# Kernel tuning notes

Hardware: AMD Instinct MI355X
Metric: run time of the kernel (lower is better)

The kernel has to match this reference:

```python
import jax, jax.numpy as jnp
import numpy as np

TAU = 2.0       # LIF membrane time constant
V_TH = 1.0      # spike threshold
ALPHA = 2.0     # ATan surrogate sharpness
EPS = 1e-5      # BatchNorm eps


@jax.custom_vjp
def spike_fn(x):
    return (x >= 0.0).astype(x.dtype)

def _spike_fwd(x):
    return spike_fn(x), x

def _spike_bwd(x, g):
    # ATan surrogate: alpha/2 / (1 + (pi/2 * alpha * x)^2)
    sg = (ALPHA / 2.0) / (1.0 + (jnp.pi / 2.0 * ALPHA * x) ** 2)
    return (g * sg,)

spike_fn.defvjp(_spike_fwd, _spike_bwd)


def lif_multistep(x):
    # x: [T, B, C, L]; spikingjelly LIFNode, decay_input=True, hard reset to 0,
    # detach_reset=True (spike detached in the reset path only).
    def step(v, xt):
        v = v + (xt - v) / TAU
        s = spike_fn(v - V_TH)
        v = (1.0 - jax.lax.stop_gradient(s)) * v
        return v, s
    v0 = jnp.zeros_like(x[0])
    _, spks = jax.lax.scan(step, v0, x)
    return spks  # [T, B, C, L]


def delta_encoder(inputs, bn_gamma, bn_beta, enc_w, enc_b):
    # inputs: [B, L, C]
    delta = jnp.concatenate(
        [jnp.zeros_like(inputs[:, :1]), inputs[:, 1:] - inputs[:, :-1]], axis=1
    )  # [B, L, C]
    d = jnp.transpose(delta, (0, 2, 1))[:, None]  # [B, 1, C, L]
    # BatchNorm2d(1), training mode: stats over all elements (single channel)
    mean = jnp.mean(d)
    var = jnp.var(d)
    d = (d - mean) * jax.lax.rsqrt(var + EPS) * bn_gamma[0] + bn_beta[0]
    d = jnp.transpose(d, (0, 2, 3, 1))  # [B, C, L, 1]
    # Linear(1, T): enc[b,c,l,t] = d[b,c,l,0] * w[t,0] + b[t]
    enc = d * enc_w[:, 0] + enc_b  # [B, C, L, T]
    enc = jnp.transpose(enc, (3, 0, 1, 2))  # [T, B, C, L]
    spks = lif_multistep(enc)
    return jnp.transpose(spks, (1, 0, 2, 3))  # [B, T, C, L]


def setup_inputs() -> dict:
    key = jax.random.key(0)
    k1, k2, k3 = jax.random.split(key, 3)
    B, L, C, T = 32, 4096, 8, 64
    inputs = jax.random.normal(k1, (B, L, C), dtype=jnp.float32)
    bn_gamma = jnp.ones((1,), dtype=jnp.float32)
    bn_beta = jnp.zeros((1,), dtype=jnp.float32)
    # torch Linear(1, T) init: U(-1, 1) since fan_in = 1
    enc_w = jax.random.uniform(k2, (T, 1), dtype=jnp.float32, minval=-1.0, maxval=1.0)
    enc_b = jax.random.uniform(k3, (T,), dtype=jnp.float32, minval=-1.0, maxval=1.0)
    return {"inputs": inputs, "bn_gamma": bn_gamma, "bn_beta": bn_beta,
            "enc_w": enc_w, "enc_b": enc_b}


def reference(inputs, bn_gamma, bn_beta, enc_w, enc_b):
    return delta_encoder(inputs, bn_gamma, bn_beta, enc_w, enc_b)
```

## Files before the change

### kernel.cpp

```cpp
#include <hip/hip_runtime.h>
#include <math.h>

#define NBATCH 32
#define NL     4096
#define NC     8
#define NT     64
#define NTOT   (NBATCH * NL * NC)

typedef float f32x4 __attribute__((ext_vector_type(4)));

__global__ __launch_bounds__(256) void reduce_kernel(const float* __restrict__ in,
                                                     double* __restrict__ part) {
    __shared__ double sm[256], sm2[256];
    const int tid = threadIdx.x;
    double s = 0.0, s2 = 0.0;
    for (int i = blockIdx.x * 256 + tid; i < NTOT; i += 256 * 256) {
        double d = 0.0;
        if ((i & (NL * NC - 1)) >= NC) {
            d = (double)in[i] - (double)in[i - NC];
        }
        s  += d;
        s2 += d * d;
    }
    sm[tid] = s; sm2[tid] = s2;
    __syncthreads();
    for (int off = 128; off > 0; off >>= 1) {
        if (tid < off) { sm[tid] += sm[tid + off]; sm2[tid] += sm2[tid + off]; }
        __syncthreads();
    }
    if (tid == 0) {
        part[2 * blockIdx.x]     = sm[0];
        part[2 * blockIdx.x + 1] = sm2[0];
    }
}

__global__ __launch_bounds__(256) void finalize_kernel(const double* __restrict__ part,
                                                       const float* __restrict__ gamma,
                                                       const float* __restrict__ beta,
                                                       const float* __restrict__ wv,
                                                       const float* __restrict__ bv,
                                                       double2* __restrict__ pq) {
    __shared__ double sm[256], sm2[256];
    __shared__ double sAB[2];
    const int tid = threadIdx.x;
    sm[tid]  = part[2 * tid];
    sm2[tid] = part[2 * tid + 1];
    __syncthreads();
    for (int off = 128; off > 0; off >>= 1) {
        if (tid < off) { sm[tid] += sm[tid + off]; sm2[tid] += sm2[tid + off]; }
        __syncthreads();
    }
    if (tid == 0) {
        const double mean = sm[0] / (double)NTOT;
        const double var  = sm2[0] / (double)NTOT - mean * mean;
        const double inv  = 1.0 / sqrt(var + 1e-5);
        const double A    = inv * (double)gamma[0];
        const double Bc   = (double)beta[0] - mean * A;
        sAB[0] = A;
        sAB[1] = Bc;
    }
    __syncthreads();
    if (tid < NT) {
        const double A  = sAB[0];
        const double Bc = sAB[1];
        const double w  = (double)wv[tid];
        const double b  = (double)bv[tid];
        double2 r;
        r.x = 0.5 * A * w;
        r.y = 0.5 * (Bc * w + b);
        pq[tid] = r;
    }
}

__global__ __launch_bounds__(256) void lif_kernel(const float* __restrict__ in,
                                                  const double2* __restrict__ pq,
                                                  float* __restrict__ out) {
    __shared__ __align__(16) double2 spq[NT];
    const int tid = threadIdx.x;
    if (tid < NT) spq[tid] = pq[tid];
    __syncthreads();

    const int blk   = blockIdx.x;
    const int chunk = blk & 3;
    const int bc    = blk >> 2;
    const int c     = bc & 7;
    const int b     = bc >> 3;
    const int l     = chunk * 1024 + tid * 4;

    const float* base = in + (b * NL + l) * NC + c;
    const float p0 = (l == 0) ? 0.0f : base[-NC];
    const float c0 = base[0];
    const float c1 = base[NC];
    const float c2 = base[2 * NC];
    const float c3 = base[3 * NC];

    double dl0 = (l == 0) ? 0.0 : ((double)c0 - (double)p0);
    double dl1 = (double)c1 - (double)c0;
    double dl2 = (double)c2 - (double)c1;
    double dl3 = (double)c3 - (double)c2;

    double v0 = 0.0, v1 = 0.0, v2 = 0.0, v3 = 0.0;
    f32x4* obase = reinterpret_cast<f32x4*>(out + ((b * NT) * NC + c) * NL + l);

#pragma unroll
    for (int t = 0; t < NT; t++) {
        const double2 PQ = spq[t];
        f32x4 o;
        double vv;
        bool s;

        vv = fma(v0, 0.5, fma(dl0, PQ.x, PQ.y));
        s = vv >= 1.0; o.x = s ? 1.0f : 0.0f; v0 = s ? 0.0 : vv;

        vv = fma(v1, 0.5, fma(dl1, PQ.x, PQ.y));
        s = vv >= 1.0; o.y = s ? 1.0f : 0.0f; v1 = s ? 0.0 : vv;

        vv = fma(v2, 0.5, fma(dl2, PQ.x, PQ.y));
        s = vv >= 1.0; o.z = s ? 1.0f : 0.0f; v2 = s ? 0.0 : vv;

        vv = fma(v3, 0.5, fma(dl3, PQ.x, PQ.y));
        s = vv >= 1.0; o.w = s ? 1.0f : 0.0f; v3 = s ? 0.0 : vv;

        __builtin_nontemporal_store(o, obase + t * (NC * NL / 4));
    }
}

extern "C" void kernel_launch(void* const* d_in, const int* in_sizes, int n_in,
                              void* d_out, int out_size, void* d_ws, size_t ws_size,
                              hipStream_t stream) {
    const float* inputs = (const float*)d_in[0];
    const float* gamma  = (const float*)d_in[1];
    const float* beta   = (const float*)d_in[2];
    const float* enc_w  = (const float*)d_in[3];
    const float* enc_b  = (const float*)d_in[4];
    float* out = (float*)d_out;

    double*  part = (double*)d_ws;
    double2* pq   = (double2*)(part + 512);

    reduce_kernel  <<<256, 256, 0, stream>>>(inputs, part);
    finalize_kernel<<<1,   256, 0, stream>>>(part, gamma, beta, enc_w, enc_b, pq);
    lif_kernel     <<<1024, 256, 0, stream>>>(inputs, pq, out);
}
```

Measured before the change: 294.3 us.

## Vectorize delta reduction loads and halve per-thread LIF work with more blocks

The reduction kernel now reads float4 vectors and their predecessor vector (8 floats back) so each thread handles four deltas per iteration, cutting load instructions. The LIF kernel is split across twice as many blocks, with each thread computing two sequence positions instead of four, storing float2 with regular (not nontemporal) stores and partial unrolling. This raises parallelism and occupancy for the double-precision recurrence, at the cost of narrower 8-byte stores and losing the nontemporal hint on the large output write.

Result: faster. 269.2 us, median of 2 (-8.5%).

```diff
diff --git a/kernel.cpp b/kernel.cpp
--- a/kernel.cpp
+++ b/kernel.cpp
@@ -13,14 +13,20 @@
                                                      double* __restrict__ part) {
     __shared__ double sm[256], sm2[256];
     const int tid = threadIdx.x;
+    const f32x4* in4 = reinterpret_cast<const f32x4*>(in);
     double s = 0.0, s2 = 0.0;
-    for (int i = blockIdx.x * 256 + tid; i < NTOT; i += 256 * 256) {
-        double d = 0.0;
-        if ((i & (NL * NC - 1)) >= NC) {
-            d = (double)in[i] - (double)in[i - NC];
+    for (int g = blockIdx.x * 256 + tid; g < NTOT / 4; g += 256 * 256) {
+        const int e = g * 4;
+        if ((e & (NL * NC - 1)) >= NC) {
+            const f32x4 cur = in4[g];
+            const f32x4 prv = in4[g - 2];
+            const double d0 = (double)cur.x - (double)prv.x;
+            const double d1 = (double)cur.y - (double)prv.y;
+            const double d2 = (double)cur.z - (double)prv.z;
+            const double d3 = (double)cur.w - (double)prv.w;
+            s  += d0 + d1 + d2 + d3;
+            s2 += d0 * d0 + d1 * d1 + d2 * d2 + d3 * d3;
         }
-        s  += d;
-        s2 += d * d;
     }
     sm[tid] = s; sm2[tid] = s2;
     __syncthreads();
@@ -81,31 +87,27 @@
     __syncthreads();
 
     const int blk   = blockIdx.x;
-    const int chunk = blk & 3;
-    const int bc    = blk >> 2;
+    const int chunk = blk & 7;
+    const int bc    = blk >> 3;
     const int c     = bc & 7;
     const int b     = bc >> 3;
-    const int l     = chunk * 1024 + tid * 4;
+    const int l     = chunk * 512 + tid * 2;
 
     const float* base = in + (b * NL + l) * NC + c;
     const float p0 = (l == 0) ? 0.0f : base[-NC];
     const float c0 = base[0];
     const float c1 = base[NC];
-    const float c2 = base[2 * NC];
-    const float c3 = base[3 * NC];
 
-    double dl0 = (l == 0) ? 0.0 : ((double)c0 - (double)p0);
-    double dl1 = (double)c1 - (double)c0;
-    double dl2 = (double)c2 - (double)c1;
-    double dl3 = (double)c3 - (double)c2;
+    const double dl0 = (l == 0) ? 0.0 : ((double)c0 - (double)p0);
+    const double dl1 = (double)c1 - (double)c0;
 
-    double v0 = 0.0, v1 = 0.0, v2 = 0.0, v3 = 0.0;
-    f32x4* obase = reinterpret_cast<f32x4*>(out + ((b * NT) * NC + c) * NL + l);
+    double v0 = 0.0, v1 = 0.0;
+    float2* obase = reinterpret_cast<float2*>(out + ((b * NT) * NC + c) * NL + l);
 
-#pragma unroll
+#pragma unroll 8
     for (int t = 0; t < NT; t++) {
         const double2 PQ = spq[t];
-        f32x4 o;
+        float2 o;
         double vv;
         bool s;
 
@@ -115,13 +117,7 @@
         vv = fma(v1, 0.5, fma(dl1, PQ.x, PQ.y));
         s = vv >= 1.0; o.y = s ? 1.0f : 0.0f; v1 = s ? 0.0 : vv;
 
-        vv = fma(v2, 0.5, fma(dl2, PQ.x, PQ.y));
-        s = vv >= 1.0; o.z = s ? 1.0f : 0.0f; v2 = s ? 0.0 : vv;
-
-        vv = fma(v3, 0.5, fma(dl3, PQ.x, PQ.y));
-        s = vv >= 1.0; o.w = s ? 1.0f : 0.0f; v3 = s ? 0.0 : vv;
-
-        __builtin_nontemporal_store(o, obase + t * (NC * NL / 4));
+        obase[t * (NC * NL / 2)] = o;
     }
 }
 
@@ -138,7 +134,7 @@
     double*  part = (double*)d_ws;
     double2* pq   = (double2*)(part + 512);
 
-    reduce_kernel  <<<256, 256, 0, stream>>>(inputs, part);
-    finalize_kernel<<<1,   256, 0, stream>>>(part, gamma, beta, enc_w, enc_b, pq);
-    lif_kernel     <<<1024, 256, 0, stream>>>(inputs, pq, out);
+    reduce_kernel  <<<256,  256, 0, stream>>>(inputs, part);
+    finalize_kernel<<<1,    256, 0, stream>>>(part, gamma, beta, enc_w, enc_b, pq);
+    lif_kernel     <<<2048, 256, 0, stream>>>(inputs, pq, out);
 }
```
